# Kernel optimization log

Hardware: AMD Instinct MI355X
Metric: run time of the kernel (lower is better)

Reference implementation:

```python
import jax, jax.numpy as jnp
import numpy as np

B, N, D, H, HD, T, E = 8, 8192, 1536, 4, 256, 50, 64
LN_EPS = 1e-5


def setup_inputs() -> dict:
    key = jax.random.key(0)
    ks = jax.random.split(key, 24)
    w = lambda k, shape, sc=0.02: (jax.random.normal(k, shape, jnp.float32) * sc)
    return {
        'features': jax.random.normal(ks[0], (B, N, D), jnp.float32),
        'attn_mask': jnp.ones((B, N), dtype=bool),
        'tissue_id': jax.random.randint(ks[1], (B,), 0, T),
        # ABMIL params (heads stacked on leading axis)
        'attW': w(ks[2], (H, D, HD)), 'attb': jnp.zeros((H, HD), jnp.float32),
        'gateW': w(ks[3], (H, D, HD)), 'gateb': jnp.zeros((H, HD), jnp.float32),
        'brW': w(ks[4], (H, HD)), 'brb': jnp.zeros((H,), jnp.float32),
        'condW': w(ks[5], (H * D, D)), 'condb': jnp.zeros((D,), jnp.float32),
        # shared feature extractor: Linear(D,256) + LayerNorm(256)
        'sfW': w(ks[6], (D, 256)), 'sfb': jnp.zeros((256,), jnp.float32),
        'sfg': jnp.ones((256,), jnp.float32), 'sfbeta': jnp.zeros((256,), jnp.float32),
        # hypernetwork: Embedding(T,E) -> Linear(E,64) -> GELU -> Linear(64,257)
        'temb': w(ks[7], (T, E), 1.0),
        'h1W': w(ks[8], (E, 64)), 'h1b': jnp.zeros((64,), jnp.float32),
        'h2W': w(ks[9], (64, 257), 0.001), 'h2b': jnp.zeros((257,), jnp.float32),
    }


def _layernorm(x, g, b):
    mu = jnp.mean(x, axis=-1, keepdims=True)
    var = jnp.mean((x - mu) ** 2, axis=-1, keepdims=True)
    return (x - mu) * jax.lax.rsqrt(var + LN_EPS) * g + b


def reference(features, attn_mask, tissue_id, attW, attb, gateW, gateb,
              brW, brb, condW, condb, sfW, sfb, sfg, sfbeta,
              temb, h1W, h1b, h2W, h2b):
    # --- ABMIL gated multi-head tanh-attention pooling (dropout is eval/no-op) ---
    a = jnp.tanh(jnp.einsum('bnd,hdk->bhnk', features, attW) + attb[:, None, :])      # [B,H,N,HD]
    g = jax.nn.sigmoid(jnp.einsum('bnd,hdk->bhnk', features, gateW) + gateb[:, None, :])
    scores = jnp.einsum('bhnk,hk->bhn', a * g, brW) + brb[None, :, None]               # [B,H,N]
    scores = jnp.where(attn_mask[:, None, :], scores, jnp.float32(-1e9))
    attn = jax.nn.softmax(scores, axis=-1)                                             # over instances
    pooled = jnp.einsum('bhn,bnd->bhd', attn, features).reshape(B, H * D)              # concat heads
    M = pooled @ condW + condb                                                          # [B,D]

    # --- shared feature extractor ---
    sh = jax.nn.gelu(_layernorm(M @ sfW + sfb, sfg, sfbeta), approximate=False)         # [B,256]

    # --- tissue hypernetwork: per-sample dynamic linear head ---
    te = temb[tissue_id]                                                                # [B,E]
    hp = jax.nn.gelu(te @ h1W + h1b, approximate=False) @ h2W + h2b                     # [B,257]
    y_pred = jnp.sum(sh * hp[:, :256], axis=-1) + hp[:, 256]                            # [B]

    head_attentions = scores[:, None, :, :]                                             # [B,1,H,N] (b r h n)
    return y_pred, head_attentions
```

## Files before the change

kernel.cpp:

```cpp
#include <hip/hip_runtime.h>


typedef unsigned short u16;
typedef unsigned int u32;
typedef __attribute__((ext_vector_type(8))) short bf16x8;
typedef __attribute__((ext_vector_type(4))) float f32x4;
typedef __attribute__((ext_vector_type(4))) float float4v;
typedef __attribute__((ext_vector_type(4))) u16 u16x4;

__device__ __forceinline__ u16 f2bf(float x) {
  u32 u = __float_as_uint(x);
  u32 r = (u + 0x7fffu + ((u >> 16) & 1u)) >> 16;
  return (u16)r;
}
__device__ __forceinline__ float bf2f(u16 v) { return __uint_as_float(((u32)v) << 16); }

__device__ __forceinline__ void async_copy16(void* lds, const void* g) {
  __builtin_amdgcn_global_load_lds((const __attribute__((address_space(1))) u32*)g,
                                   (__attribute__((address_space(3))) u32*)lds, 16, 0, 0);
}
__device__ __forceinline__ float fsigm(float x) { return 1.f / (1.f + __expf(-x)); }
__device__ __forceinline__ float ftanh(float x) {
  x = fminf(fmaxf(x, -15.f), 15.f);
  float e = __expf(2.f * x);
  return (e - 1.f) / (e + 1.f);
}
__device__ __forceinline__ float gelu_exact(float x) {
  return 0.5f * x * (1.f + erff(x * 0.70710678118654752f));
}


__global__ void zero_kernel(float* __restrict__ p, int n) {
  int i = blockIdx.x * 256 + threadIdx.x;
  if (i < n) p[i] = 0.f;
}

__global__ void convert_kernel(const float* __restrict__ f, u16* __restrict__ o, long n4) {
  long stride = (long)gridDim.x * blockDim.x;
  for (long i = blockIdx.x * (long)blockDim.x + threadIdx.x; i < n4; i += stride) {
    float4v v = ((const float4v*)f)[i];
    u16x4 r;
    r[0] = f2bf(v[0]); r[1] = f2bf(v[1]); r[2] = f2bf(v[2]); r[3] = f2bf(v[3]);
    ((u16x4*)o)[i] = r;
  }
}

__global__ void pack_kernel(const float* __restrict__ attW, const float* __restrict__ gateW,
                            u16* __restrict__ Bp) {
  int idx = blockIdx.x * 256 + threadIdx.x;
  int c = idx / 393216;
  int r = idx - c * 393216;
  int col = r / 1536;
  int d = r - col * 1536;
  int h = c >> 1;
  int k = ((c & 1) << 7) + (col >> 1);
  const float* W = (col & 1) ? gateW : attW;
  Bp[idx] = f2bf(W[(h * 1536 + d) * 256 + k]);
}

__global__ __launch_bounds__(256, 4)
void gemm_scores_kernel(const u16* __restrict__ A, const u16* __restrict__ Bp,
                        const float* __restrict__ attb, const float* __restrict__ gateb,
                        const float* __restrict__ brW, float* __restrict__ scores)
{
  __shared__ u16 Al[128 * 64];
  __shared__ u16 Bl[128 * 64];

  const int tid = threadIdx.x;
  const int lane = tid & 63;
  const int wid = tid >> 6;
  const int wm = wid >> 1;
  const int wn = wid & 1;
  const int tileM = blockIdx.x >> 4;
  const int panel = blockIdx.x & 15;

  const int srow = tid >> 3;
  const int sk8 = (tid & 7) ^ (srow & 7);
  const u16* aSrc = A + ((long)(tileM * 128 + srow)) * 1536 + sk8 * 8;
  const u16* bSrc = Bp + (long)panel * 196608 + (long)srow * 1536 + sk8 * 8;
  u16* aDst = Al + tid * 8;
  u16* bDst = Bl + tid * 8;

  int aOff[2][4], bOff[2][4];
#pragma unroll
  for (int s = 0; s < 2; ++s) {
#pragma unroll
    for (int m = 0; m < 4; ++m) {
      int r = wm * 64 + m * 16 + (lane & 15);
      aOff[s][m] = r * 64 + (((s * 4 + (lane >> 4)) ^ (r & 7)) << 3);
    }
#pragma unroll
    for (int n = 0; n < 4; ++n) {
      int c = wn * 64 + n * 16 + (lane & 15);
      bOff[s][n] = c * 64 + (((s * 4 + (lane >> 4)) ^ (c & 7)) << 3);
    }
  }

  f32x4 acc[4][4] = {};

  for (int kt = 0; kt < 24; ++kt) {
    const int off = kt * 64;
#pragma unroll
    for (int j = 0; j < 4; ++j)
      async_copy16(aDst + j * 2048, aSrc + (long)j * 32 * 1536 + off);
#pragma unroll
    for (int j = 0; j < 4; ++j)
      async_copy16(bDst + j * 2048, bSrc + (long)j * 32 * 1536 + off);
    __syncthreads();
#pragma unroll
    for (int s = 0; s < 2; ++s) {
      bf16x8 bfr[4], af[4];
#pragma unroll
      for (int n = 0; n < 4; ++n) bfr[n] = *(const bf16x8*)&Bl[bOff[s][n]];
#pragma unroll
      for (int m = 0; m < 4; ++m) af[m] = *(const bf16x8*)&Al[aOff[s][m]];
#pragma unroll
      for (int m = 0; m < 4; ++m)
#pragma unroll
        for (int n = 0; n < 4; ++n)
          acc[m][n] = __builtin_amdgcn_mfma_f32_16x16x32_bf16(af[m], bfr[n], acc[m][n], 0, 0, 0);
    }
    __syncthreads();
  }

  float brw[4], bia[4];
  int par[4];
#pragma unroll
  for (int n = 0; n < 4; ++n) {
    int g = panel * 128 + wn * 64 + n * 16 + (lane & 15);
    int h_ = g >> 9;
    int k = (((g >> 8) & 1) << 7) + ((g & 255) >> 1);
    par[n] = g & 1;
    brw[n] = brW[h_ * 256 + k];
    bia[n] = par[n] ? gateb[h_ * 256 + k] : attb[h_ * 256 + k];
  }
  const int hh = (panel * 128) >> 9;
#pragma unroll
  for (int m = 0; m < 4; ++m) {
#pragma unroll
    for (int i = 0; i < 4; ++i) {
      float s = 0.f;
#pragma unroll
      for (int n = 0; n < 4; ++n) {
        float v = acc[m][n][i] + bia[n];
        float t = par[n] ? fsigm(v) : ftanh(v);
        float tp = __shfl_xor(t, 1);
        s += par[n] ? 0.f : t * tp * brw[n];
      }
      s += __shfl_xor(s, 1);
      s += __shfl_xor(s, 2);
      s += __shfl_xor(s, 4);
      s += __shfl_xor(s, 8);
      if ((lane & 15) == 0) {
        int row = tileM * 128 + wm * 64 + m * 16 + ((lane >> 4) << 2) + i;
        int b = row >> 13;
        int n_ = row & 8191;
        atomicAdd(&scores[((b << 2) + hh) * 8192 + n_], s);
      }
    }
  }
}

__global__ __launch_bounds__(512)
void softmax_kernel(const float* __restrict__ scores, const float* __restrict__ brb,
                    float* __restrict__ attn, float* __restrict__ ha)
{
  const int bh = blockIdx.x;
  const float bb = brb[bh & 3];
  const long base = (long)bh * 8192;
  const int t = threadIdx.x;
  const int lane = t & 63, wid = t >> 6;
  __shared__ float red[8];
  float v[16];
  float mx = -1e30f;
#pragma unroll
  for (int i = 0; i < 16; ++i) {
    v[i] = scores[base + t + i * 512] + bb;
    mx = fmaxf(mx, v[i]);
  }
#pragma unroll
  for (int o = 1; o < 64; o <<= 1) mx = fmaxf(mx, __shfl_xor(mx, o));
  if (lane == 0) red[wid] = mx;
  __syncthreads();
#pragma unroll
  for (int w = 0; w < 8; ++w) mx = fmaxf(mx, red[w]);
  __syncthreads();
  float sum = 0.f;
#pragma unroll
  for (int i = 0; i < 16; ++i) {
    float sc = v[i];
    ha[base + t + i * 512] = sc;
    float e = __expf(sc - mx);
    v[i] = e;
    sum += e;
  }
#pragma unroll
  for (int o = 1; o < 64; o <<= 1) sum += __shfl_xor(sum, o);
  if (lane == 0) red[wid] = sum;
  __syncthreads();
  sum = 0.f;
#pragma unroll
  for (int w = 0; w < 8; ++w) sum += red[w];
  float inv = 1.f / sum;
#pragma unroll
  for (int i = 0; i < 16; ++i) attn[base + t + i * 512] = v[i] * inv;
}

__global__ __launch_bounds__(384)
void pooled_kernel(const u16* __restrict__ fbf, const float* __restrict__ attn,
                   float* __restrict__ pooled)
{
  __shared__ float aw[4][256];
  const int t = threadIdx.x;
  const int b = blockIdx.x >> 5;
  const int nc = blockIdx.x & 31;
  for (int i = t; i < 1024; i += 384)
    aw[i >> 8][i & 255] = attn[((b << 2) + (i >> 8)) * 8192 + nc * 256 + (i & 255)];
  __syncthreads();
  float acc[4][4] = {};
  const u16* basep = fbf + ((long)(b * 8192 + nc * 256)) * 1536 + t * 4;
  for (int n = 0; n < 256; ++n) {
    u16x4 v = *(const u16x4*)(basep + (long)n * 1536);
    float a0 = aw[0][n], a1 = aw[1][n], a2 = aw[2][n], a3 = aw[3][n];
#pragma unroll
    for (int j = 0; j < 4; ++j) {
      float f = bf2f(v[j]);
      acc[j][0] += a0 * f;
      acc[j][1] += a1 * f;
      acc[j][2] += a2 * f;
      acc[j][3] += a3 * f;
    }
  }
#pragma unroll
  for (int j = 0; j < 4; ++j)
#pragma unroll
    for (int h = 0; h < 4; ++h)
      atomicAdd(&pooled[((b << 2) + h) * 1536 + t * 4 + j], acc[j][h]);
}

__global__ __launch_bounds__(256)
void cond_kernel(const float* __restrict__ pooled, const float* __restrict__ condW,
                 const float* __restrict__ condb, float* __restrict__ M)
{
  __shared__ float pl[8 * 192];
  const int t = threadIdx.x;
  const int dc = blockIdx.x % 6;
  const int ks = blockIdx.x / 6;
  const int k0 = ks * 192;
  for (int i = t; i < 8 * 192; i += 256) {
    int b = i / 192, kk = i - b * 192;
    pl[i] = pooled[b * 6144 + k0 + kk];
  }
  __syncthreads();
  const int d = dc * 256 + t;
  float acc[8] = {};
  for (int kk = 0; kk < 192; ++kk) {
    float w = condW[(long)(k0 + kk) * 1536 + d];
#pragma unroll
    for (int b = 0; b < 8; ++b) acc[b] += pl[b * 192 + kk] * w;
  }
  if (ks == 0) {
    float cb = condb[d];
#pragma unroll
    for (int b = 0; b < 8; ++b) acc[b] += cb;
  }
#pragma unroll
  for (int b = 0; b < 8; ++b) atomicAdd(&M[b * 1536 + d], acc[b]);
}

__global__ __launch_bounds__(256)
void sf_kernel(const float* __restrict__ M, const float* __restrict__ sfW,
               const float* __restrict__ sfb, const float* __restrict__ sfg,
               const float* __restrict__ sfbeta, float* __restrict__ sh)
{
  __shared__ float mr[1536];
  __shared__ float red[4];
  const int b = blockIdx.x;
  const int c = threadIdx.x;
  const int lane = c & 63, wid = c >> 6;
  for (int i = c; i < 1536; i += 256) mr[i] = M[b * 1536 + i];
  __syncthreads();
  float acc = sfb[c];
  for (int k = 0; k < 1536; ++k) acc += mr[k] * sfW[k * 256 + c];
  float s = acc;
#pragma unroll
  for (int o = 1; o < 64; o <<= 1) s += __shfl_xor(s, o);
  if (lane == 0) red[wid] = s;
  __syncthreads();
  float mu = (red[0] + red[1] + red[2] + red[3]) * (1.f / 256.f);
  __syncthreads();
  float dv = (acc - mu) * (acc - mu);
#pragma unroll
  for (int o = 1; o < 64; o <<= 1) dv += __shfl_xor(dv, o);
  if (lane == 0) red[wid] = dv;
  __syncthreads();
  float var = (red[0] + red[1] + red[2] + red[3]) * (1.f / 256.f);
  float xn = (acc - mu) * rsqrtf(var + 1e-5f) * sfg[c] + sfbeta[c];
  sh[b * 256 + c] = gelu_exact(xn);
}

__global__ __launch_bounds__(320)
void head_kernel(const float* __restrict__ sh, const int* __restrict__ tissue,
                 const float* __restrict__ temb, const float* __restrict__ h1W,
                 const float* __restrict__ h1b, const float* __restrict__ h2W,
                 const float* __restrict__ h2b, float* __restrict__ y)
{
  __shared__ float hid[64];
  __shared__ float hp[257];
  __shared__ float red[5];
  const int t = threadIdx.x;
  const int lane = t & 63, wid = t >> 6;
  for (int b = 0; b < 8; ++b) {
    const int tix = tissue[b];
    if (t < 64) {
      float s = h1b[t];
      for (int e = 0; e < 64; ++e) s += temb[tix * 64 + e] * h1W[e * 64 + t];
      hid[t] = gelu_exact(s);
    }
    __syncthreads();
    if (t < 257) {
      float s = h2b[t];
      for (int j = 0; j < 64; ++j) s += hid[j] * h2W[j * 257 + t];
      hp[t] = s;
    }
    __syncthreads();
    float p = (t < 256) ? sh[b * 256 + t] * hp[t] : 0.f;
#pragma unroll
    for (int o = 1; o < 64; o <<= 1) p += __shfl_xor(p, o);
    if (lane == 0) red[wid] = p;
    __syncthreads();
    if (t == 0) y[b] = red[0] + red[1] + red[2] + red[3] + red[4] + hp[256];
    __syncthreads();
  }
}


extern "C" void kernel_launch(void* const* d_in, const int* in_sizes, int n_in,
                              void* d_out, int out_size, void* d_ws, size_t ws_size,
                              hipStream_t stream) {
  const float* features = (const float*)d_in[0];
  const int* tissue     = (const int*)d_in[2];
  const float* attW     = (const float*)d_in[3];
  const float* attb     = (const float*)d_in[4];
  const float* gateW    = (const float*)d_in[5];
  const float* gateb    = (const float*)d_in[6];
  const float* brW      = (const float*)d_in[7];
  const float* brb      = (const float*)d_in[8];
  const float* condW    = (const float*)d_in[9];
  const float* condb    = (const float*)d_in[10];
  const float* sfW      = (const float*)d_in[11];
  const float* sfb      = (const float*)d_in[12];
  const float* sfg      = (const float*)d_in[13];
  const float* sfbeta   = (const float*)d_in[14];
  const float* temb     = (const float*)d_in[15];
  const float* h1W      = (const float*)d_in[16];
  const float* h1b      = (const float*)d_in[17];
  const float* h2W      = (const float*)d_in[18];
  const float* h2b      = (const float*)d_in[19];

  char* ws = (char*)d_ws;
  u16* fbf      = (u16*)ws;
  u16* Bp       = (u16*)(ws + 201326592);
  float* scores = (float*)(ws + 207618048);
  float* pooled = (float*)(ws + 208666624);
  float* Mbuf   = (float*)(ws + 208863232);
  float* attn   = (float*)(ws + 208912384);
  float* shb    = (float*)(ws + 209960960);

  float* yout = (float*)d_out;
  float* haout = (float*)d_out + 8;

  zero_kernel<<<1264, 256, 0, stream>>>(scores, 323584);
  convert_kernel<<<2048, 256, 0, stream>>>(features, fbf, 25165824L);
  pack_kernel<<<12288, 256, 0, stream>>>(attW, gateW, Bp);
  gemm_scores_kernel<<<8192, 256, 0, stream>>>(fbf, Bp, attb, gateb, brW, scores);
  softmax_kernel<<<32, 512, 0, stream>>>(scores, brb, attn, haout);
  pooled_kernel<<<256, 384, 0, stream>>>(fbf, attn, pooled);
  cond_kernel<<<192, 256, 0, stream>>>(pooled, condW, condb, Mbuf);
  sf_kernel<<<8, 256, 0, stream>>>(Mbuf, sfW, sfb, sfg, sfbeta, shb);
  head_kernel<<<1, 320, 0, stream>>>(shb, tissue, temb, h1W, h1b, h2W, h2b, yout);
}
```

Measured before the change: 780.9 us.

## Use 32x32 MFMA in scores GEMM, merge prep kernels, parallelize head per batch

The scores GEMM switches from 16x16x32 to 32x32x16 bf16 MFMA tiles, with the LDS offsets and epilogue row mapping adjusted. This cuts LDS fragment loads per MFMA and may raise math throughput. The zero, convert and pack kernels are merged into one prep launch, and the head kernel now runs one block per batch instead of a serial loop. The epilogue needs a wider shuffle reduction, and the larger accumulators could raise register pressure.

```diff
diff --git a/kernel.cpp b/kernel.cpp
--- a/kernel.cpp
+++ b/kernel.cpp
@@ -4,7 +4,7 @@
 typedef unsigned short u16;
 typedef unsigned int u32;
 typedef __attribute__((ext_vector_type(8))) short bf16x8;
-typedef __attribute__((ext_vector_type(4))) float f32x4;
+typedef __attribute__((ext_vector_type(16))) float f32x16;
 typedef __attribute__((ext_vector_type(4))) float float4v;
 typedef __attribute__((ext_vector_type(4))) u16 u16x4;
 
@@ -29,33 +29,34 @@
   return 0.5f * x * (1.f + erff(x * 0.70710678118654752f));
 }
 
-
-__global__ void zero_kernel(float* __restrict__ p, int n) {
-  int i = blockIdx.x * 256 + threadIdx.x;
-  if (i < n) p[i] = 0.f;
-}
-
-__global__ void convert_kernel(const float* __restrict__ f, u16* __restrict__ o, long n4) {
-  long stride = (long)gridDim.x * blockDim.x;
-  for (long i = blockIdx.x * (long)blockDim.x + threadIdx.x; i < n4; i += stride) {
-    float4v v = ((const float4v*)f)[i];
-    u16x4 r;
-    r[0] = f2bf(v[0]); r[1] = f2bf(v[1]); r[2] = f2bf(v[2]); r[3] = f2bf(v[3]);
-    ((u16x4*)o)[i] = r;
-  }
-}
-
-__global__ void pack_kernel(const float* __restrict__ attW, const float* __restrict__ gateW,
-                            u16* __restrict__ Bp) {
-  int idx = blockIdx.x * 256 + threadIdx.x;
-  int c = idx / 393216;
-  int r = idx - c * 393216;
-  int col = r / 1536;
-  int d = r - col * 1536;
-  int h = c >> 1;
-  int k = ((c & 1) << 7) + (col >> 1);
-  const float* W = (col & 1) ? gateW : attW;
-  Bp[idx] = f2bf(W[(h * 1536 + d) * 256 + k]);
+__global__ void prep_kernel(const float* __restrict__ attW, const float* __restrict__ gateW,
+                            u16* __restrict__ Bp, const float* __restrict__ f,
+                            u16* __restrict__ o, float* __restrict__ zp) {
+  const int bid = blockIdx.x;
+  const int tid = threadIdx.x;
+  if (bid < 12288) {
+    int idx = bid * 256 + tid;
+    int c = idx / 393216;
+    int r = idx - c * 393216;
+    int col = r / 1536;
+    int d = r - col * 1536;
+    int h = c >> 1;
+    int k = ((c & 1) << 7) + (col >> 1);
+    const float* W = (col & 1) ? gateW : attW;
+    Bp[idx] = f2bf(W[(h * 1536 + d) * 256 + k]);
+  } else if (bid < 14336) {
+    const long n4 = 25165824L;
+    const long stride = 2048L * 256L;
+    for (long i = (long)(bid - 12288) * 256 + tid; i < n4; i += stride) {
+      float4v v = ((const float4v*)f)[i];
+      u16x4 r;
+      r[0] = f2bf(v[0]); r[1] = f2bf(v[1]); r[2] = f2bf(v[2]); r[3] = f2bf(v[3]);
+      ((u16x4*)o)[i] = r;
+    }
+  } else {
+    int i = (bid - 14336) * 256 + tid;
+    if (i < 323584) zp[i] = 0.f;
+  }
 }
 
 __global__ __launch_bounds__(256, 4)
@@ -81,78 +82,76 @@
   u16* aDst = Al + tid * 8;
   u16* bDst = Bl + tid * 8;
 
-  int aOff[2][4], bOff[2][4];
-#pragma unroll
-  for (int s = 0; s < 2; ++s) {
-#pragma unroll
-    for (int m = 0; m < 4; ++m) {
-      int r = wm * 64 + m * 16 + (lane & 15);
-      aOff[s][m] = r * 64 + (((s * 4 + (lane >> 4)) ^ (r & 7)) << 3);
-    }
-#pragma unroll
-    for (int n = 0; n < 4; ++n) {
-      int c = wn * 64 + n * 16 + (lane & 15);
-      bOff[s][n] = c * 64 + (((s * 4 + (lane >> 4)) ^ (c & 7)) << 3);
-    }
-  }
-
-  f32x4 acc[4][4] = {};
+  int aOff[4][2], bOff[4][2];
+#pragma unroll
+  for (int s = 0; s < 4; ++s) {
+#pragma unroll
+    for (int mi = 0; mi < 2; ++mi) {
+      int r = wm * 64 + mi * 32 + (lane & 31);
+      aOff[s][mi] = r * 64 + (((s * 2 + (lane >> 5)) ^ (r & 7)) << 3);
+    }
+#pragma unroll
+    for (int ni = 0; ni < 2; ++ni) {
+      int c = wn * 64 + ni * 32 + (lane & 31);
+      bOff[s][ni] = c * 64 + (((s * 2 + (lane >> 5)) ^ (c & 7)) << 3);
+    }
+  }
+
+  f32x16 acc[2][2] = {};
 
   for (int kt = 0; kt < 24; ++kt) {
     const int off = kt * 64;
 #pragma unroll
     for (int j = 0; j < 4; ++j)
-      async_copy16(aDst + j * 2048, aSrc + (long)j * 32 * 1536 + off);
+      async_copy16(aDst + j * 2048, aSrc + (long)(j * 32) * 1536 + off);
 #pragma unroll
     for (int j = 0; j < 4; ++j)
-      async_copy16(bDst + j * 2048, bSrc + (long)j * 32 * 1536 + off);
+      async_copy16(bDst + j * 2048, bSrc + (long)(j * 32) * 1536 + off);
     __syncthreads();
 #pragma unroll
-    for (int s = 0; s < 2; ++s) {
-      bf16x8 bfr[4], af[4];
-#pragma unroll
-      for (int n = 0; n < 4; ++n) bfr[n] = *(const bf16x8*)&Bl[bOff[s][n]];
-#pragma unroll
-      for (int m = 0; m < 4; ++m) af[m] = *(const bf16x8*)&Al[aOff[s][m]];
-#pragma unroll
-      for (int m = 0; m < 4; ++m)
-#pragma unroll
-        for (int n = 0; n < 4; ++n)
-          acc[m][n] = __builtin_amdgcn_mfma_f32_16x16x32_bf16(af[m], bfr[n], acc[m][n], 0, 0, 0);
+    for (int s = 0; s < 4; ++s) {
+      bf16x8 a0 = *(const bf16x8*)&Al[aOff[s][0]];
+      bf16x8 a1 = *(const bf16x8*)&Al[aOff[s][1]];
+      bf16x8 b0 = *(const bf16x8*)&Bl[bOff[s][0]];
+      bf16x8 b1 = *(const bf16x8*)&Bl[bOff[s][1]];
+      acc[0][0] = __builtin_amdgcn_mfma_f32_32x32x16_bf16(a0, b0, acc[0][0], 0, 0, 0);
+      acc[0][1] = __builtin_amdgcn_mfma_f32_32x32x16_bf16(a0, b1, acc[0][1], 0, 0, 0);
+      acc[1][0] = __builtin_amdgcn_mfma_f32_32x32x16_bf16(a1, b0, acc[1][0], 0, 0, 0);
+      acc[1][1] = __builtin_amdgcn_mfma_f32_32x32x16_bf16(a1, b1, acc[1][1], 0, 0, 0);
     }
     __syncthreads();
   }
 
-  float brw[4], bia[4];
-  int par[4];
-#pragma unroll
-  for (int n = 0; n < 4; ++n) {
-    int g = panel * 128 + wn * 64 + n * 16 + (lane & 15);
+  float brw[2], bia[2];
+  const int par = lane & 1;
+#pragma unroll
+  for (int n = 0; n < 2; ++n) {
+    int g = panel * 128 + wn * 64 + n * 32 + (lane & 31);
     int h_ = g >> 9;
     int k = (((g >> 8) & 1) << 7) + ((g & 255) >> 1);
-    par[n] = g & 1;
     brw[n] = brW[h_ * 256 + k];
-    bia[n] = par[n] ? gateb[h_ * 256 + k] : attb[h_ * 256 + k];
-  }
-  const int hh = (panel * 128) >> 9;
-#pragma unroll
-  for (int m = 0; m < 4; ++m) {
-#pragma unroll
-    for (int i = 0; i < 4; ++i) {
+    bia[n] = par ? gateb[h_ * 256 + k] : attb[h_ * 256 + k];
+  }
+  const int hh = panel >> 2;
+#pragma unroll
+  for (int mi = 0; mi < 2; ++mi) {
+#pragma unroll
+    for (int i = 0; i < 16; ++i) {
       float s = 0.f;
 #pragma unroll
-      for (int n = 0; n < 4; ++n) {
-        float v = acc[m][n][i] + bia[n];
-        float t = par[n] ? fsigm(v) : ftanh(v);
+      for (int n = 0; n < 2; ++n) {
+        float v = acc[mi][n][i] + bia[n];
+        float t = par ? fsigm(v) : ftanh(v);
         float tp = __shfl_xor(t, 1);
-        s += par[n] ? 0.f : t * tp * brw[n];
+        s += par ? 0.f : t * tp * brw[n];
       }
       s += __shfl_xor(s, 1);
       s += __shfl_xor(s, 2);
       s += __shfl_xor(s, 4);
       s += __shfl_xor(s, 8);
-      if ((lane & 15) == 0) {
-        int row = tileM * 128 + wm * 64 + m * 16 + ((lane >> 4) << 2) + i;
+      s += __shfl_xor(s, 16);
+      if ((lane & 31) == 0) {
+        int row = tileM * 128 + wm * 64 + mi * 32 + (i & 3) + 8 * (i >> 2) + 4 * (lane >> 5);
         int b = row >> 13;
         int n_ = row & 8191;
         atomicAdd(&scores[((b << 2) + hh) * 8192 + n_], s);
@@ -310,28 +309,26 @@
   __shared__ float red[5];
   const int t = threadIdx.x;
   const int lane = t & 63, wid = t >> 6;
-  for (int b = 0; b < 8; ++b) {
-    const int tix = tissue[b];
-    if (t < 64) {
-      float s = h1b[t];
-      for (int e = 0; e < 64; ++e) s += temb[tix * 64 + e] * h1W[e * 64 + t];
-      hid[t] = gelu_exact(s);
-    }
-    __syncthreads();
-    if (t < 257) {
-      float s = h2b[t];
-      for (int j = 0; j < 64; ++j) s += hid[j] * h2W[j * 257 + t];
-      hp[t] = s;
-    }
-    __syncthreads();
-    float p = (t < 256) ? sh[b * 256 + t] * hp[t] : 0.f;
-#pragma unroll
-    for (int o = 1; o < 64; o <<= 1) p += __shfl_xor(p, o);
-    if (lane == 0) red[wid] = p;
-    __syncthreads();
-    if (t == 0) y[b] = red[0] + red[1] + red[2] + red[3] + red[4] + hp[256];
-    __syncthreads();
-  }
+  const int b = blockIdx.x;
+  const int tix = tissue[b];
+  if (t < 64) {
+    float s = h1b[t];
+    for (int e = 0; e < 64; ++e) s += temb[tix * 64 + e] * h1W[e * 64 + t];
+    hid[t] = gelu_exact(s);
+  }
+  __syncthreads();
+  if (t < 257) {
+    float s = h2b[t];
+    for (int j = 0; j < 64; ++j) s += hid[j] * h2W[j * 257 + t];
+    hp[t] = s;
+  }
+  __syncthreads();
+  float p = (t < 256) ? sh[b * 256 + t] * hp[t] : 0.f;
+#pragma unroll
+  for (int o = 1; o < 64; o <<= 1) p += __shfl_xor(p, o);
+  if (lane == 0) red[wid] = p;
+  __syncthreads();
+  if (t == 0) y[b] = red[0] + red[1] + red[2] + red[3] + red[4] + hp[256];
 }
 
 
@@ -370,13 +367,11 @@
   float* yout = (float*)d_out;
   float* haout = (float*)d_out + 8;
 
-  zero_kernel<<<1264, 256, 0, stream>>>(scores, 323584);
-  convert_kernel<<<2048, 256, 0, stream>>>(features, fbf, 25165824L);
-  pack_kernel<<<12288, 256, 0, stream>>>(attW, gateW, Bp);
+  prep_kernel<<<15600, 256, 0, stream>>>(attW, gateW, Bp, features, fbf, scores);
   gemm_scores_kernel<<<8192, 256, 0, stream>>>(fbf, Bp, attb, gateb, brW, scores);
   softmax_kernel<<<32, 512, 0, stream>>>(scores, brb, attn, haout);
   pooled_kernel<<<256, 384, 0, stream>>>(fbf, attn, pooled);
   cond_kernel<<<192, 256, 0, stream>>>(pooled, condW, condb, Mbuf);
   sf_kernel<<<8, 256, 0, stream>>>(Mbuf, sfW, sfb, sfg, sfbeta, shb);
-  head_kernel<<<1, 320, 0, stream>>>(shb, tissue, temb, h1W, h1b, h2W, h2b, yout);
-}
+  head_kernel<<<8, 320, 0, stream>>>(shb, tissue, temb, h1W, h1b, h2W, h2b, yout);
+}
```

Result: no change. 778.0 us (-0.4%).
